# Optimization experiments

Measured on AMD Instinct MI355X. Metric: run time of the kernel, lower is better.

## Reference

```python
import jax, jax.numpy as jnp
import numpy as np

EPS = 1e-5
NUM_HEADS = 16


def layernorm(x, g, b):
    m = jnp.mean(x, axis=-1, keepdims=True)
    v = jnp.mean(jnp.square(x - m), axis=-1, keepdims=True)
    return (x - m) * jax.lax.rsqrt(v + EPS) * g + b


def setup_inputs() -> dict:
    key = jax.random.key(0)
    ks = jax.random.split(key, 8)
    B, S, E, F = 16, 512, 1024, 4096
    s_e = 1.0 / np.sqrt(E)
    s_f = 1.0 / np.sqrt(F)
    return {
        "input": jax.random.normal(ks[0], (B, S, E), jnp.float32),
        "ln1_g": jnp.ones((E,), jnp.float32),
        "ln1_b": jnp.zeros((E,), jnp.float32),
        "wq": jax.random.normal(ks[1], (E, E), jnp.float32) * s_e,
        "bq": jnp.zeros((E,), jnp.float32),
        "wk": jax.random.normal(ks[2], (E, E), jnp.float32) * s_e,
        "bk": jnp.zeros((E,), jnp.float32),
        "wv": jax.random.normal(ks[3], (E, E), jnp.float32) * s_e,
        "bv": jnp.zeros((E,), jnp.float32),
        "wo": jax.random.normal(ks[4], (E, E), jnp.float32) * s_e,
        "bo": jnp.zeros((E,), jnp.float32),
        "ln2_g": jnp.ones((E,), jnp.float32),
        "ln2_b": jnp.zeros((E,), jnp.float32),
        "w1": jax.random.normal(ks[5], (E, F), jnp.float32) * s_e,
        "b1": jnp.zeros((F,), jnp.float32),
        "w2": jax.random.normal(ks[6], (F, E), jnp.float32) * s_f,
        "b2": jnp.zeros((E,), jnp.float32),
    }


def attention(x, wq, bq, wk, bk, wv, bv, wo, bo):
    B, S, E = x.shape
    H = NUM_HEADS
    D = E // H
    q = (x @ wq + bq).reshape(B, S, H, D)
    k = (x @ wk + bk).reshape(B, S, H, D)
    v = (x @ wv + bv).reshape(B, S, H, D)
    scores = jnp.einsum("bqhd,bkhd->bhqk", q, k) * (1.0 / np.sqrt(D))
    attn = jax.nn.softmax(scores, axis=-1)
    out = jnp.einsum("bhqk,bkhd->bqhd", attn, v).reshape(B, S, E)
    return out @ wo + bo


def reference(input, ln1_g, ln1_b, wq, bq, wk, bk, wv, bv, wo, bo,
              ln2_g, ln2_b, w1, b1, w2, b2):
    # pre-LN attention + residual
    x = layernorm(input, ln1_g, ln1_b)
    x = attention(x, wq, bq, wk, bk, wv, bv, wo, bo)
    x = x + input
    # pre-LN MLP (GELU exact, matching nn.GELU default) + residual
    y = layernorm(x, ln2_g, ln2_b)
    y = jax.nn.gelu(y @ w1 + b1, approximate=False)
    y = y @ w2 + b2
    return x + y
```

## Files before the change

kernel.cpp:

```cpp
#include <hip/hip_runtime.h>
#include <hip/hip_bf16.h>


typedef __bf16 bf16x8 __attribute__((ext_vector_type(8)));
typedef __bf16 bf16x4 __attribute__((ext_vector_type(4)));
typedef float  f32x4  __attribute__((ext_vector_type(4)));

#define EPI_QKV  0
#define EPI_RES  1
#define EPI_GELU 2

__device__ __forceinline__ void async_copy16(const void* g, void* l) {
  __builtin_amdgcn_global_load_lds((const __attribute__((address_space(1))) void*)g,
                                   (__attribute__((address_space(3))) void*)l, 16, 0, 0);
}

__global__ __launch_bounds__(256) void prep_weights(
    const float* __restrict__ wq, const float* __restrict__ wk,
    const float* __restrict__ wv, const float* __restrict__ wo,
    const float* __restrict__ w1, const float* __restrict__ w2,
    const float* __restrict__ bq, const float* __restrict__ bk,
    const float* __restrict__ bv,
    __bf16* __restrict__ wqkvT, __bf16* __restrict__ woT,
    __bf16* __restrict__ w1T, __bf16* __restrict__ w2T, float* __restrict__ bqkv) {
  const int bid = blockIdx.x;
  if (bid >= 12288) {
    const int i = (bid - 12288) * 256 + threadIdx.x;
    bqkv[i] = (i < 1024) ? bq[i] : ((i < 2048) ? bk[i - 1024] : bv[i - 2048]);
    return;
  }
  const float* in;
  __bf16* out;
  int K, N, tile;
  if (bid < 4096) {
    const int w = bid >> 10;
    tile = bid & 1023;
    in = (w == 0) ? wq : (w == 1) ? wk : (w == 2) ? wv : wo;
    out = (w == 3) ? woT : (wqkvT + (size_t)w * 1024 * 1024);
    K = 1024; N = 1024;
  } else if (bid < 8192) { tile = bid - 4096; in = w1; out = w1T; K = 1024; N = 4096; }
  else                   { tile = bid - 8192; in = w2; out = w2T; K = 4096; N = 1024; }
  const int ntx = N >> 5;
  const int bx = tile % ntx, by = tile / ntx;
  const int n0 = bx * 32, k0 = by * 32;

  __shared__ float tilebuf[32][33];
  const int tx = threadIdx.x & 31, ty = threadIdx.x >> 5;
#pragma unroll
  for (int i = 0; i < 4; i++)
    tilebuf[ty + i * 8][tx] = in[(size_t)(k0 + ty + i * 8) * N + n0 + tx];
  __syncthreads();
#pragma unroll
  for (int i = 0; i < 4; i++)
    out[(size_t)(n0 + ty + i * 8) * K + k0 + tx] = (__bf16)tilebuf[tx][ty + i * 8];
}

__device__ __forceinline__ float block_sum(float v, float* red) {
#pragma unroll
  for (int off = 32; off; off >>= 1) v += __shfl_down(v, off);
  const int w = threadIdx.x >> 6;
  __syncthreads();
  if ((threadIdx.x & 63) == 0) red[w] = v;
  __syncthreads();
  return red[0] + red[1] + red[2] + red[3];
}

__global__ __launch_bounds__(256) void ln_kernel(const float* __restrict__ x,
                                                 const float* __restrict__ g,
                                                 const float* __restrict__ bta,
                                                 __bf16* __restrict__ out) {
  __shared__ float red[8];
  const int row = blockIdx.x, t = threadIdx.x;
  const float4 v = ((const float4*)(x + (size_t)row * 1024))[t];
  float s = v.x + v.y + v.z + v.w;
  s = block_sum(s, red);
  const float mean = s * (1.0f / 1024.0f);
  const float d0 = v.x - mean, d1 = v.y - mean, d2 = v.z - mean, d3 = v.w - mean;
  float vs = d0 * d0 + d1 * d1 + d2 * d2 + d3 * d3;
  vs = block_sum(vs, red);
  const float rstd = rsqrtf(vs * (1.0f / 1024.0f) + 1e-5f);
  const float4 gg = ((const float4*)g)[t];
  const float4 bb = ((const float4*)bta)[t];
  bf16x4 o;
  o[0] = (__bf16)(d0 * rstd * gg.x + bb.x);
  o[1] = (__bf16)(d1 * rstd * gg.y + bb.y);
  o[2] = (__bf16)(d2 * rstd * gg.z + bb.z);
  o[3] = (__bf16)(d3 * rstd * gg.w + bb.w);
  ((bf16x4*)out)[(size_t)row * 256 + t] = o;
}

template <int EPI>
__global__ __launch_bounds__(256, 2) void gemm_bt(const __bf16* __restrict__ A,
                                                  const __bf16* __restrict__ Bt,
                                                  const float* __restrict__ bias,
                                                  const float* __restrict__ res,
                                                  void* __restrict__ out,
                                                  void* __restrict__ out2,
                                                  int N, int K) {
  __shared__ __bf16 lA[128 * 64];
  __shared__ __bf16 lB[128 * 64];
  const int t = threadIdx.x;
  const int wave = t >> 6, lane = t & 63;
  const int lm = lane & 15, lq = lane >> 4;

  const int Ntiles = gridDim.x;
  const int flat = blockIdx.y * Ntiles + blockIdx.x;
  const int xcd = flat & 7;
  const int local = flat >> 3;
  const int tn = local % Ntiles;
  const int tm = (local / Ntiles) * 8 + xcd;
  const int m0 = tm * 128, n0 = tn * 128;
  const int wm = (wave & 1) * 64, wn = (wave >> 1) * 64;

  f32x4 acc[4][4] = {};

  const int srow = t >> 3, sslot = t & 7;
  const int schunk = sslot ^ (srow & 7);
  const __bf16* aSrc = A + (size_t)(m0 + srow) * K + schunk * 8;
  const __bf16* bSrc = Bt + (size_t)(n0 + srow) * K + schunk * 8;

  for (int k0 = 0; k0 < K; k0 += 64) {
#pragma unroll
    for (int i = 0; i < 4; i++) {
      async_copy16(aSrc + (size_t)(i * 32) * K, lA + i * 2048 + t * 8);
      async_copy16(bSrc + (size_t)(i * 32) * K, lB + i * 2048 + t * 8);
    }
    aSrc += 64; bSrc += 64;
    __syncthreads();
#pragma unroll
    for (int kk = 0; kk < 2; kk++) {
      bf16x8 af[4], bf[4];
      const int slot = (kk * 4 + lq) ^ (lm & 7);
#pragma unroll
      for (int i = 0; i < 4; i++) {
        af[i] = *(const bf16x8*)&lA[(wm + i * 16 + lm) * 64 + slot * 8];
        bf[i] = *(const bf16x8*)&lB[(wn + i * 16 + lm) * 64 + slot * 8];
      }
#pragma unroll
      for (int mi = 0; mi < 4; mi++)
#pragma unroll
        for (int ni = 0; ni < 4; ni++)
          acc[mi][ni] = __builtin_amdgcn_mfma_f32_16x16x32_bf16(af[mi], bf[ni], acc[mi][ni], 0, 0, 0);
    }
    __syncthreads();
  }

#pragma unroll
  for (int mi = 0; mi < 4; mi++) {
    const int gr = m0 + wm + mi * 16 + lq * 4;
#pragma unroll
    for (int ni = 0; ni < 4; ni++) {
      const int gc = n0 + wn + ni * 16 + lm;
      const float bv = bias[gc];
#pragma unroll
      for (int r = 0; r < 4; r++) {
        float v = acc[mi][ni][r] + bv;
        const int row = gr + r;
        if (EPI == EPI_GELU) {
          v = 0.5f * v * (1.0f + erff(v * 0.70710678118654752f));
          ((__bf16*)out)[(size_t)row * N + gc] = (__bf16)v;
        } else if (EPI == EPI_RES) {
          ((float*)out)[(size_t)row * N + gc] = v + res[(size_t)row * N + gc];
        } else {
          if (gc < 2048) {
            ((__bf16*)out)[(size_t)row * 2048 + gc] = (__bf16)v;
          } else {
            const int d = gc & 63, hh = (gc - 2048) >> 6;
            const int bb = row >> 9, ss = row & 511;
            ((__bf16*)out2)[(((size_t)bb * 16 + hh) * 64 + d) * 512 + ss] = (__bf16)v;
          }
        }
      }
    }
  }
}

#define MFMA_QUAD(MI0)                                                         \
  do {                                                                         \
    _Pragma("unroll") for (int kk = 0; kk < 2; ++kk) {                         \
      _Pragma("unroll") for (int ni = 0; ni < 4; ++ni) {                       \
        acc[MI0][ni] = __builtin_amdgcn_mfma_f32_16x16x32_bf16(                \
            af[MI0][kk], bf[ni][kk], acc[MI0][ni], 0, 0, 0);                   \
        acc[(MI0) + 1][ni] = __builtin_amdgcn_mfma_f32_16x16x32_bf16(          \
            af[(MI0) + 1][kk], bf[ni][kk], acc[(MI0) + 1][ni], 0, 0, 0);       \
      }                                                                        \
    }                                                                          \
  } while (0)

#define READ_A(MI)                                                             \
  _Pragma("unroll") for (int kk = 0; kk < 2; ++kk)                             \
      af[MI][kk] = *(const bf16x8*)&bufA[(wm * 128 + (MI)*16 + lm) * 64 +      \
                                         (((kk * 4 + lq) ^ sw) * 8)];

template <int EPI>
__global__ __launch_bounds__(512, 2) void gemm8_bt(const __bf16* __restrict__ A,
                                                   const __bf16* __restrict__ Bt,
                                                   const float* __restrict__ bias,
                                                   void* __restrict__ out,
                                                   void* __restrict__ out2,
                                                   int N, int K) {
  __shared__ __bf16 lA[2 * 256 * 64];
  __shared__ __bf16 lB[2 * 256 * 64];
  const int t = threadIdx.x;
  const int wave = t >> 6, lane = t & 63;
  const int lm = lane & 15, lq = lane >> 4, sw = lm & 7;
  const int wm = wave >> 2, wn = wave & 3;

  const int Ntiles = gridDim.x;
  const int flat = blockIdx.y * Ntiles + blockIdx.x;
  const int xcd = flat & 7;
  const int local = flat >> 3;
  const int tn = local % Ntiles;
  const int tm = (local / Ntiles) * 8 + xcd;
  const int m0 = tm * 256, n0 = tn * 256;

  const int NT = K >> 6;

  const int srow = t >> 3;
  const int schunk = (t & 7) ^ (srow & 7);
  const __bf16* aBase = A + (size_t)(m0 + srow) * K + schunk * 8;
  const __bf16* bBase = Bt + (size_t)(n0 + srow) * K + schunk * 8;
  __bf16* ldA = lA + t * 8;
  __bf16* ldB = lB + t * 8;

  auto stage = [&](int h) {
    if (h >= 4 * NT) return;
    const int tau = h >> 2, type = h & 3, hf = type & 1;
    const size_t roff = (size_t)(hf * 128) * K + (size_t)tau * 64;
    const int loff = (tau & 1) * 16384 + hf * 8192;
    if (type < 2) {
      async_copy16(aBase + roff, ldA + loff);
      async_copy16(aBase + roff + (size_t)64 * K, ldA + loff + 4096);
    } else {
      async_copy16(bBase + roff, ldB + loff);
      async_copy16(bBase + roff + (size_t)64 * K, ldB + loff + 4096);
    }
  };

  f32x4 acc[8][4] = {};

  for (int h = 0; h < 6; ++h) stage(h);
  asm volatile("s_waitcnt vmcnt(4)" ::: "memory");
  __builtin_amdgcn_s_barrier();

  for (int tt = 0; tt < NT; ++tt) {
    const __bf16* bufA = lA + (tt & 1) * 16384;
    const __bf16* bufB = lB + (tt & 1) * 16384;
    bf16x8 af[8][2], bf[4][2];

#pragma unroll
    for (int ni = 0; ni < 4; ++ni)
#pragma unroll
      for (int kk = 0; kk < 2; ++kk)
        bf[ni][kk] = *(const bf16x8*)&bufB[(wn * 64 + ni * 16 + lm) * 64 +
                                           (((kk * 4 + lq) ^ sw) * 8)];
    READ_A(0)
    READ_A(1)
    stage(4 * tt + 6);
    __builtin_amdgcn_s_barrier();
    asm volatile("s_waitcnt lgkmcnt(0)" ::: "memory");
    __builtin_amdgcn_sched_barrier(0);
    __builtin_amdgcn_s_setprio(1);
    MFMA_QUAD(0);
    __builtin_amdgcn_s_setprio(0);
    __builtin_amdgcn_s_barrier();

    READ_A(2)
    READ_A(3)
    READ_A(4)
    READ_A(5)
    READ_A(6)
    READ_A(7)
    stage(4 * tt + 7);
    __builtin_amdgcn_s_barrier();
    asm volatile("s_waitcnt lgkmcnt(0)" ::: "memory");
    __builtin_amdgcn_sched_barrier(0);
    __builtin_amdgcn_s_setprio(1);
    MFMA_QUAD(2);
    __builtin_amdgcn_s_setprio(0);
    __builtin_amdgcn_s_barrier();

    stage(4 * tt + 8);
    __builtin_amdgcn_s_barrier();
    __builtin_amdgcn_s_setprio(1);
    MFMA_QUAD(4);
    __builtin_amdgcn_s_setprio(0);
    __builtin_amdgcn_s_barrier();

    stage(4 * tt + 9);
    __builtin_amdgcn_s_barrier();
    __builtin_amdgcn_s_setprio(1);
    MFMA_QUAD(6);
    __builtin_amdgcn_s_setprio(0);

    if (tt < NT - 1) {
      if (tt == NT - 2) asm volatile("s_waitcnt vmcnt(0)" ::: "memory");
      else              asm volatile("s_waitcnt vmcnt(4)" ::: "memory");
      __builtin_amdgcn_s_barrier();
    }
  }

#pragma unroll
  for (int mi = 0; mi < 8; ++mi) {
    const int gr = m0 + wm * 128 + mi * 16 + lq * 4;
#pragma unroll
    for (int ni = 0; ni < 4; ++ni) {
      const int gc = n0 + wn * 64 + ni * 16 + lm;
      const float bv = bias[gc];
#pragma unroll
      for (int r = 0; r < 4; ++r) {
        float v = acc[mi][ni][r] + bv;
        const int row = gr + r;
        if (EPI == EPI_GELU) {
          v = 0.5f * v * (1.0f + erff(v * 0.70710678118654752f));
          ((__bf16*)out)[(size_t)row * N + gc] = (__bf16)v;
        } else {
          if (gc < 2048) {
            ((__bf16*)out)[(size_t)row * 2048 + gc] = (__bf16)v;
          } else {
            const int d = gc & 63, hh = (gc - 2048) >> 6;
            const int bb = row >> 9, ss = row & 511;
            ((__bf16*)out2)[(((size_t)bb * 16 + hh) * 64 + d) * 512 + ss] = (__bf16)v;
          }
        }
      }
    }
  }
}

__global__ __launch_bounds__(256) void attn_kernel(const __bf16* __restrict__ qk,
                                                   const __bf16* __restrict__ Vt,
                                                   __bf16* __restrict__ outA) {
  __shared__ __bf16 lK[128 * 64];
  __shared__ __bf16 lV[64 * 128];
  __shared__ __bf16 lP[4][16 * 128];
  const int t = threadIdx.x, wave = t >> 6, lane = t & 63;
  const int lm = lane & 15, lq = lane >> 4;
  const int sw = lm & 7;
  const int flat = blockIdx.x;
  const int xcd = flat & 7, local = flat >> 3;
  const int qt = local & 7;
  const int bh = (local >> 3) * 8 + xcd;
  const int h = bh & 15, b = bh >> 4;
  const int q0 = qt * 64 + wave * 16;

  const size_t qrow = (size_t)(b * 512 + q0 + lm) * 2048 + h * 64;
  bf16x8 aq0 = *(const bf16x8*)&qk[qrow + lq * 8];
  bf16x8 aq1 = *(const bf16x8*)&qk[qrow + 32 + lq * 8];

  float mrow[4] = {-3e38f, -3e38f, -3e38f, -3e38f};
  float lrow[4] = {0.f, 0.f, 0.f, 0.f};
  f32x4 o[4] = {};

  const int krow = t >> 3;
  const int kchunk = (t & 7) ^ (krow & 7);
  const __bf16* kSrc = qk + (size_t)(b * 512 + krow) * 2048 + 1024 + h * 64 + kchunk * 8;
  const int vrow = t >> 4;
  const int vchunk = (t & 15) ^ (vrow & 7);
  const __bf16* vSrc = Vt + ((size_t)bh * 64 + vrow) * 512 + vchunk * 8;

  for (int kt = 0; kt < 4; kt++) {
#pragma unroll
    for (int i = 0; i < 4; i++) {
      async_copy16(kSrc + (size_t)(kt * 128 + i * 32) * 2048, lK + i * 2048 + t * 8);
      async_copy16(vSrc + kt * 128 + (size_t)(i * 16) * 512, lV + i * 2048 + t * 8);
    }
    __syncthreads();

    f32x4 s[8];
#pragma unroll
    for (int ni = 0; ni < 8; ni++) {
      bf16x8 bk0 = *(const bf16x8*)&lK[(ni * 16 + lm) * 64 + ((lq ^ sw) * 8)];
      bf16x8 bk1 = *(const bf16x8*)&lK[(ni * 16 + lm) * 64 + (((4 + lq) ^ sw) * 8)];
      f32x4 z = {};
      z = __builtin_amdgcn_mfma_f32_16x16x32_bf16(aq0, bk0, z, 0, 0, 0);
      z = __builtin_amdgcn_mfma_f32_16x16x32_bf16(aq1, bk1, z, 0, 0, 0);
      s[ni] = z;
    }
#pragma unroll
    for (int ni = 0; ni < 8; ni++)
#pragma unroll
      for (int r = 0; r < 4; r++) s[ni][r] *= 0.125f;

    float mnew[4], alpha[4];
#pragma unroll
    for (int r = 0; r < 4; r++) {
      float mx = s[0][r];
#pragma unroll
      for (int ni = 1; ni < 8; ni++) mx = fmaxf(mx, s[ni][r]);
#pragma unroll
      for (int off = 1; off < 16; off <<= 1) mx = fmaxf(mx, __shfl_xor(mx, off));
      mnew[r] = fmaxf(mrow[r], mx);
      alpha[r] = __expf(mrow[r] - mnew[r]);
      mrow[r] = mnew[r];
    }
    float rs[4] = {0.f, 0.f, 0.f, 0.f};
#pragma unroll
    for (int ni = 0; ni < 8; ni++)
#pragma unroll
      for (int r = 0; r < 4; r++) {
        const float p = __expf(s[ni][r] - mnew[r]);
        s[ni][r] = p;
        rs[r] += p;
      }
#pragma unroll
    for (int r = 0; r < 4; r++) {
#pragma unroll
      for (int off = 1; off < 16; off <<= 1) rs[r] += __shfl_xor(rs[r], off);
      lrow[r] = lrow[r] * alpha[r] + rs[r];
    }

#pragma unroll
    for (int ni = 0; ni < 8; ni++) {
      const int chunk = ni * 2 + (lm >> 3);
#pragma unroll
      for (int r = 0; r < 4; r++) {
        const int q = lq * 4 + r;
        lP[wave][q * 128 + ((chunk ^ (q & 7)) * 8) + (lm & 7)] = (__bf16)s[ni][r];
      }
    }
    asm volatile("s_waitcnt lgkmcnt(0)" ::: "memory");
    bf16x8 ap[4];
#pragma unroll
    for (int kc = 0; kc < 4; kc++)
      ap[kc] = *(const bf16x8*)&lP[wave][lm * 128 + (((kc * 4 + lq) ^ sw) * 8)];

#pragma unroll
    for (int di = 0; di < 4; di++)
#pragma unroll
      for (int r = 0; r < 4; r++) o[di][r] *= alpha[r];

#pragma unroll
    for (int di = 0; di < 4; di++) {
#pragma unroll
      for (int kc = 0; kc < 4; kc++) {
        bf16x8 bv = *(const bf16x8*)&lV[(di * 16 + lm) * 128 + (((kc * 4 + lq) ^ sw) * 8)];
        o[di] = __builtin_amdgcn_mfma_f32_16x16x32_bf16(ap[kc], bv, o[di], 0, 0, 0);
      }
    }
    __syncthreads();
  }

#pragma unroll
  for (int di = 0; di < 4; di++)
#pragma unroll
    for (int r = 0; r < 4; r++) {
      const float v = o[di][r] / lrow[r];
      outA[(size_t)(b * 512 + q0 + lq * 4 + r) * 1024 + h * 64 + di * 16 + lm] = (__bf16)v;
    }
}

extern "C" void kernel_launch(void* const* d_in, const int* in_sizes, int n_in,
                              void* d_out, int out_size, void* d_ws, size_t ws_size,
                              hipStream_t stream) {
  const float* input = (const float*)d_in[0];
  const float* ln1_g = (const float*)d_in[1];
  const float* ln1_b = (const float*)d_in[2];
  const float* wq = (const float*)d_in[3];
  const float* bq = (const float*)d_in[4];
  const float* wk = (const float*)d_in[5];
  const float* bk = (const float*)d_in[6];
  const float* wv = (const float*)d_in[7];
  const float* bv = (const float*)d_in[8];
  const float* wo = (const float*)d_in[9];
  const float* bo = (const float*)d_in[10];
  const float* ln2_g = (const float*)d_in[11];
  const float* ln2_b = (const float*)d_in[12];
  const float* w1 = (const float*)d_in[13];
  const float* b1 = (const float*)d_in[14];
  const float* w2 = (const float*)d_in[15];
  const float* b2 = (const float*)d_in[16];

  char* ws = (char*)d_ws;
  __bf16* wqkvT = (__bf16*)(ws + 0);
  __bf16* woT   = (__bf16*)(ws + ((size_t)6 << 20));
  __bf16* w1T   = (__bf16*)(ws + ((size_t)8 << 20));
  __bf16* w2T   = (__bf16*)(ws + ((size_t)16 << 20));
  __bf16* qkbuf = (__bf16*)(ws + ((size_t)24 << 20));
  __bf16* vtbuf = (__bf16*)(ws + ((size_t)56 << 20));
  __bf16* abuf  = (__bf16*)(ws + ((size_t)72 << 20));
  float*  xbuf  = (float*) (ws + ((size_t)24 << 20));
  __bf16* ylnbuf= (__bf16*)(ws + ((size_t)56 << 20));
  __bf16* hbuf  = (__bf16*)(ws + ((size_t)72 << 20));
  float*  bqkv  = (float*) (ws + ((size_t)136 << 20));

  const dim3 blk(256);
  const dim3 blk8(512);
  prep_weights<<<12300, blk, 0, stream>>>(wq, wk, wv, wo, w1, w2, bq, bk, bv,
                                          wqkvT, woT, w1T, w2T, bqkv);

  ln_kernel<<<8192, blk, 0, stream>>>(input, ln1_g, ln1_b, abuf);
  gemm8_bt<EPI_QKV><<<dim3(12, 32), blk8, 0, stream>>>(abuf, wqkvT, bqkv,
                                                       qkbuf, vtbuf, 3072, 1024);
  attn_kernel<<<2048, blk, 0, stream>>>(qkbuf, vtbuf, abuf);
  gemm_bt<EPI_RES><<<dim3(8, 64), blk, 0, stream>>>(abuf, woT, bo, input,
                                                    xbuf, nullptr, 1024, 1024);
  ln_kernel<<<8192, blk, 0, stream>>>(xbuf, ln2_g, ln2_b, ylnbuf);
  gemm8_bt<EPI_GELU><<<dim3(16, 32), blk8, 0, stream>>>(ylnbuf, w1T, b1,
                                                        hbuf, nullptr, 4096, 1024);
  gemm_bt<EPI_RES><<<dim3(8, 64), blk, 0, stream>>>(hbuf, w2T, b2, xbuf,
                                                    d_out, nullptr, 1024, 4096);
}
```

Baseline: 512.9 us.

## Replace simple GEMM with pipelined 256x128 gemm4 kernel and rebalance gemm8 staging

Adds a new 512-thread gemm4_bt kernel with 256x128 tiles, double-buffered async global-to-LDS loads and phased barriers. It replaces the single-buffered 128x128 gemm_bt for the two residual GEMMs and the gemm8 kernel for the QKV projection. The gemm8 pipeline is also restaged: A tiles now load as a whole two tiles ahead, B halves load interleaved with the compute phases, and A fragment reads are spread evenly across the four phases. The aim is to hide global-load latency and balance LDS reads against MFMA work, at the cost of more LDS per block and fewer blocks in the grid for the N=1024 GEMMs.

```diff
diff --git a/kernel.cpp b/kernel.cpp
--- a/kernel.cpp
+++ b/kernel.cpp
@@ -89,92 +89,6 @@
   ((bf16x4*)out)[(size_t)row * 256 + t] = o;
 }
 
-template <int EPI>
-__global__ __launch_bounds__(256, 2) void gemm_bt(const __bf16* __restrict__ A,
-                                                  const __bf16* __restrict__ Bt,
-                                                  const float* __restrict__ bias,
-                                                  const float* __restrict__ res,
-                                                  void* __restrict__ out,
-                                                  void* __restrict__ out2,
-                                                  int N, int K) {
-  __shared__ __bf16 lA[128 * 64];
-  __shared__ __bf16 lB[128 * 64];
-  const int t = threadIdx.x;
-  const int wave = t >> 6, lane = t & 63;
-  const int lm = lane & 15, lq = lane >> 4;
-
-  const int Ntiles = gridDim.x;
-  const int flat = blockIdx.y * Ntiles + blockIdx.x;
-  const int xcd = flat & 7;
-  const int local = flat >> 3;
-  const int tn = local % Ntiles;
-  const int tm = (local / Ntiles) * 8 + xcd;
-  const int m0 = tm * 128, n0 = tn * 128;
-  const int wm = (wave & 1) * 64, wn = (wave >> 1) * 64;
-
-  f32x4 acc[4][4] = {};
-
-  const int srow = t >> 3, sslot = t & 7;
-  const int schunk = sslot ^ (srow & 7);
-  const __bf16* aSrc = A + (size_t)(m0 + srow) * K + schunk * 8;
-  const __bf16* bSrc = Bt + (size_t)(n0 + srow) * K + schunk * 8;
-
-  for (int k0 = 0; k0 < K; k0 += 64) {
-#pragma unroll
-    for (int i = 0; i < 4; i++) {
-      async_copy16(aSrc + (size_t)(i * 32) * K, lA + i * 2048 + t * 8);
-      async_copy16(bSrc + (size_t)(i * 32) * K, lB + i * 2048 + t * 8);
-    }
-    aSrc += 64; bSrc += 64;
-    __syncthreads();
-#pragma unroll
-    for (int kk = 0; kk < 2; kk++) {
-      bf16x8 af[4], bf[4];
-      const int slot = (kk * 4 + lq) ^ (lm & 7);
-#pragma unroll
-      for (int i = 0; i < 4; i++) {
-        af[i] = *(const bf16x8*)&lA[(wm + i * 16 + lm) * 64 + slot * 8];
-        bf[i] = *(const bf16x8*)&lB[(wn + i * 16 + lm) * 64 + slot * 8];
-      }
-#pragma unroll
-      for (int mi = 0; mi < 4; mi++)
-#pragma unroll
-        for (int ni = 0; ni < 4; ni++)
-          acc[mi][ni] = __builtin_amdgcn_mfma_f32_16x16x32_bf16(af[mi], bf[ni], acc[mi][ni], 0, 0, 0);
-    }
-    __syncthreads();
-  }
-
-#pragma unroll
-  for (int mi = 0; mi < 4; mi++) {
-    const int gr = m0 + wm + mi * 16 + lq * 4;
-#pragma unroll
-    for (int ni = 0; ni < 4; ni++) {
-      const int gc = n0 + wn + ni * 16 + lm;
-      const float bv = bias[gc];
-#pragma unroll
-      for (int r = 0; r < 4; r++) {
-        float v = acc[mi][ni][r] + bv;
-        const int row = gr + r;
-        if (EPI == EPI_GELU) {
-          v = 0.5f * v * (1.0f + erff(v * 0.70710678118654752f));
-          ((__bf16*)out)[(size_t)row * N + gc] = (__bf16)v;
-        } else if (EPI == EPI_RES) {
-          ((float*)out)[(size_t)row * N + gc] = v + res[(size_t)row * N + gc];
-        } else {
-          if (gc < 2048) {
-            ((__bf16*)out)[(size_t)row * 2048 + gc] = (__bf16)v;
-          } else {
-            const int d = gc & 63, hh = (gc - 2048) >> 6;
-            const int bb = row >> 9, ss = row & 511;
-            ((__bf16*)out2)[(((size_t)bb * 16 + hh) * 64 + d) * 512 + ss] = (__bf16)v;
-          }
-        }
-      }
-    }
-  }
-}
-
 #define MFMA_QUAD(MI0)                                                         \
   do {                                                                         \
     _Pragma("unroll") for (int kk = 0; kk < 2; ++kk) {                         \
@@ -187,7 +101,12 @@
     }                                                                          \
   } while (0)
 
-#define READ_A(MI)                                                             \
+#define PHASE_SYNC()                                                           \
+  __builtin_amdgcn_s_barrier();                                                \
+  asm volatile("s_waitcnt lgkmcnt(0)" ::: "memory");                           \
+  __builtin_amdgcn_sched_barrier(0)
+
+#define READ_A8(MI)                                                            \
   _Pragma("unroll") for (int kk = 0; kk < 2; ++kk)                             \
       af[MI][kk] = *(const bf16x8*)&bufA[(wm * 128 + (MI)*16 + lm) * 64 +      \
                                          (((kk * 4 + lq) ^ sw) * 8)];
@@ -220,26 +139,26 @@
   const int schunk = (t & 7) ^ (srow & 7);
   const __bf16* aBase = A + (size_t)(m0 + srow) * K + schunk * 8;
   const __bf16* bBase = Bt + (size_t)(n0 + srow) * K + schunk * 8;
-  __bf16* ldA = lA + t * 8;
-  __bf16* ldB = lB + t * 8;
-
-  auto stage = [&](int h) {
-    if (h >= 4 * NT) return;
-    const int tau = h >> 2, type = h & 3, hf = type & 1;
-    const size_t roff = (size_t)(hf * 128) * K + (size_t)tau * 64;
-    const int loff = (tau & 1) * 16384 + hf * 8192;
-    if (type < 2) {
-      async_copy16(aBase + roff, ldA + loff);
-      async_copy16(aBase + roff + (size_t)64 * K, ldA + loff + 4096);
-    } else {
-      async_copy16(bBase + roff, ldB + loff);
-      async_copy16(bBase + roff + (size_t)64 * K, ldB + loff + 4096);
-    }
+
+  auto stageA = [&](int tau) {
+    if (tau >= NT) return;
+    const __bf16* src = aBase + (size_t)tau * 64;
+    __bf16* dst = lA + (tau & 1) * 16384 + t * 8;
+#pragma unroll
+    for (int i = 0; i < 4; ++i)
+      async_copy16(src + (size_t)(i * 64) * K, dst + i * 4096);
   };
+  auto stageB = [&](int tau, int half) {
+    if (tau >= NT) return;
+    const __bf16* src = bBase + (size_t)tau * 64 + (size_t)(half * 128) * K;
+    __bf16* dst = lB + (tau & 1) * 16384 + half * 8192 + t * 8;
+    async_copy16(src, dst);
+    async_copy16(src + (size_t)64 * K, dst + 4096);
+  };
 
   f32x4 acc[8][4] = {};
 
-  for (int h = 0; h < 6; ++h) stage(h);
+  stageA(0); stageB(0, 0); stageB(0, 1); stageA(1);
   asm volatile("s_waitcnt vmcnt(4)" ::: "memory");
   __builtin_amdgcn_s_barrier();
 
@@ -254,46 +173,42 @@
       for (int kk = 0; kk < 2; ++kk)
         bf[ni][kk] = *(const bf16x8*)&bufB[(wn * 64 + ni * 16 + lm) * 64 +
                                            (((kk * 4 + lq) ^ sw) * 8)];
-    READ_A(0)
-    READ_A(1)
-    stage(4 * tt + 6);
-    __builtin_amdgcn_s_barrier();
-    asm volatile("s_waitcnt lgkmcnt(0)" ::: "memory");
-    __builtin_amdgcn_sched_barrier(0);
+    READ_A8(0)
+    READ_A8(1)
+    stageB(tt + 1, 0);
+    PHASE_SYNC();
     __builtin_amdgcn_s_setprio(1);
     MFMA_QUAD(0);
     __builtin_amdgcn_s_setprio(0);
     __builtin_amdgcn_s_barrier();
 
-    READ_A(2)
-    READ_A(3)
-    READ_A(4)
-    READ_A(5)
-    READ_A(6)
-    READ_A(7)
-    stage(4 * tt + 7);
-    __builtin_amdgcn_s_barrier();
-    asm volatile("s_waitcnt lgkmcnt(0)" ::: "memory");
-    __builtin_amdgcn_sched_barrier(0);
+    READ_A8(2)
+    READ_A8(3)
+    stageB(tt + 1, 1);
+    PHASE_SYNC();
     __builtin_amdgcn_s_setprio(1);
     MFMA_QUAD(2);
     __builtin_amdgcn_s_setprio(0);
     __builtin_amdgcn_s_barrier();
 
-    stage(4 * tt + 8);
-    __builtin_amdgcn_s_barrier();
+    READ_A8(4)
+    READ_A8(5)
+    PHASE_SYNC();
     __builtin_amdgcn_s_setprio(1);
     MFMA_QUAD(4);
     __builtin_amdgcn_s_setprio(0);
     __builtin_amdgcn_s_barrier();
 
-    stage(4 * tt + 9);
-    __builtin_amdgcn_s_barrier();
+    READ_A8(6)
+    READ_A8(7)
+    PHASE_SYNC();
     __builtin_amdgcn_s_setprio(1);
     MFMA_QUAD(6);
     __builtin_amdgcn_s_setprio(0);
+    __builtin_amdgcn_s_barrier();
 
     if (tt < NT - 1) {
+      stageA(tt + 2);
       if (tt == NT - 2) asm volatile("s_waitcnt vmcnt(0)" ::: "memory");
       else              asm volatile("s_waitcnt vmcnt(4)" ::: "memory");
       __builtin_amdgcn_s_barrier();
@@ -314,6 +229,126 @@
         if (EPI == EPI_GELU) {
           v = 0.5f * v * (1.0f + erff(v * 0.70710678118654752f));
           ((__bf16*)out)[(size_t)row * N + gc] = (__bf16)v;
+        } else {
+          if (gc < 2048) {
+            ((__bf16*)out)[(size_t)row * 2048 + gc] = (__bf16)v;
+          } else {
+            const int d = gc & 63, hh = (gc - 2048) >> 6;
+            const int bb = row >> 9, ss = row & 511;
+            ((__bf16*)out2)[(((size_t)bb * 16 + hh) * 64 + d) * 512 + ss] = (__bf16)v;
+          }
+        }
+      }
+    }
+  }
+}
+
+#define READ_A4(MI)                                                            \
+  _Pragma("unroll") for (int kk = 0; kk < 2; ++kk)                             \
+      af[MI][kk] = *(const bf16x8*)&bufA[(wm * 64 + (MI)*16 + lm) * 64 +       \
+                                         (((kk * 4 + lq) ^ sw) * 8)];
+
+template <int EPI>
+__global__ __launch_bounds__(512, 2) void gemm4_bt(const __bf16* __restrict__ A,
+                                                   const __bf16* __restrict__ Bt,
+                                                   const float* __restrict__ bias,
+                                                   const float* __restrict__ res,
+                                                   void* __restrict__ out,
+                                                   void* __restrict__ out2,
+                                                   int N, int K) {
+  __shared__ __bf16 lA[2 * 256 * 64];
+  __shared__ __bf16 lB[2 * 128 * 64];
+  const int t = threadIdx.x;
+  const int wave = t >> 6, lane = t & 63;
+  const int lm = lane & 15, lq = lane >> 4, sw = lm & 7;
+  const int wm = wave >> 1, wn = wave & 1;
+
+  const int Ntiles = gridDim.x;
+  const int flat = blockIdx.y * Ntiles + blockIdx.x;
+  const int xcd = flat & 7;
+  const int local = flat >> 3;
+  const int tn = local % Ntiles;
+  const int tm = (local / Ntiles) * 8 + xcd;
+  const int m0 = tm * 256, n0 = tn * 128;
+
+  const int NT = K >> 6;
+
+  const int srow = t >> 3;
+  const int schunk = (t & 7) ^ (srow & 7);
+  const __bf16* aBase = A + (size_t)(m0 + srow) * K + schunk * 8;
+  const __bf16* bBase = Bt + (size_t)(n0 + srow) * K + schunk * 8;
+
+  auto stageA = [&](int tau) {
+    if (tau >= NT) return;
+    const __bf16* src = aBase + (size_t)tau * 64;
+    __bf16* dst = lA + (tau & 1) * 16384 + t * 8;
+#pragma unroll
+    for (int i = 0; i < 4; ++i)
+      async_copy16(src + (size_t)(i * 64) * K, dst + i * 4096);
+  };
+  auto stageB = [&](int tau) {
+    if (tau >= NT) return;
+    const __bf16* src = bBase + (size_t)tau * 64;
+    __bf16* dst = lB + (tau & 1) * 8192 + t * 8;
+    async_copy16(src, dst);
+    async_copy16(src + (size_t)64 * K, dst + 4096);
+  };
+
+  f32x4 acc[4][4] = {};
+
+  stageA(0); stageB(0); stageA(1);
+  asm volatile("s_waitcnt vmcnt(4)" ::: "memory");
+  __builtin_amdgcn_s_barrier();
+
+  for (int tt = 0; tt < NT; ++tt) {
+    const __bf16* bufA = lA + (tt & 1) * 16384;
+    const __bf16* bufB = lB + (tt & 1) * 8192;
+    bf16x8 af[4][2], bf[4][2];
+
+#pragma unroll
+    for (int ni = 0; ni < 4; ++ni)
+#pragma unroll
+      for (int kk = 0; kk < 2; ++kk)
+        bf[ni][kk] = *(const bf16x8*)&bufB[(wn * 64 + ni * 16 + lm) * 64 +
+                                           (((kk * 4 + lq) ^ sw) * 8)];
+    READ_A4(0)
+    READ_A4(1)
+    stageB(tt + 1);
+    PHASE_SYNC();
+    __builtin_amdgcn_s_setprio(1);
+    MFMA_QUAD(0);
+    __builtin_amdgcn_s_setprio(0);
+    __builtin_amdgcn_s_barrier();
+
+    READ_A4(2)
+    READ_A4(3)
+    PHASE_SYNC();
+    __builtin_amdgcn_s_setprio(1);
+    MFMA_QUAD(2);
+    __builtin_amdgcn_s_setprio(0);
+    __builtin_amdgcn_s_barrier();
+
+    if (tt < NT - 1) {
+      stageA(tt + 2);
+      if (tt == NT - 2) asm volatile("s_waitcnt vmcnt(0)" ::: "memory");
+      else              asm volatile("s_waitcnt vmcnt(4)" ::: "memory");
+      __builtin_amdgcn_s_barrier();
+    }
+  }
+
+#pragma unroll
+  for (int mi = 0; mi < 4; ++mi) {
+    const int gr = m0 + wm * 64 + mi * 16 + lq * 4;
+#pragma unroll
+    for (int ni = 0; ni < 4; ++ni) {
+      const int gc = n0 + wn * 64 + ni * 16 + lm;
+      const float bv = bias[gc];
+#pragma unroll
+      for (int r = 0; r < 4; ++r) {
+        float v = acc[mi][ni][r] + bv;
+        const int row = gr + r;
+        if (EPI == EPI_RES) {
+          ((float*)out)[(size_t)row * N + gc] = v + res[(size_t)row * N + gc];
         } else {
           if (gc < 2048) {
             ((__bf16*)out)[(size_t)row * 2048 + gc] = (__bf16)v;
@@ -490,14 +525,14 @@
                                           wqkvT, woT, w1T, w2T, bqkv);
 
   ln_kernel<<<8192, blk, 0, stream>>>(input, ln1_g, ln1_b, abuf);
-  gemm8_bt<EPI_QKV><<<dim3(12, 32), blk8, 0, stream>>>(abuf, wqkvT, bqkv,
+  gemm4_bt<EPI_QKV><<<dim3(24, 32), blk8, 0, stream>>>(abuf, wqkvT, bqkv, nullptr,
                                                        qkbuf, vtbuf, 3072, 1024);
   attn_kernel<<<2048, blk, 0, stream>>>(qkbuf, vtbuf, abuf);
-  gemm_bt<EPI_RES><<<dim3(8, 64), blk, 0, stream>>>(abuf, woT, bo, input,
-                                                    xbuf, nullptr, 1024, 1024);
+  gemm4_bt<EPI_RES><<<dim3(8, 32), blk8, 0, stream>>>(abuf, woT, bo, input,
+                                                      xbuf, nullptr, 1024, 1024);
   ln_kernel<<<8192, blk, 0, stream>>>(xbuf, ln2_g, ln2_b, ylnbuf);
   gemm8_bt<EPI_GELU><<<dim3(16, 32), blk8, 0, stream>>>(ylnbuf, w1T, b1,
                                                         hbuf, nullptr, 4096, 1024);
-  gemm_bt<EPI_RES><<<dim3(8, 64), blk, 0, stream>>>(hbuf, w2T, b2, xbuf,
-                                                    d_out, nullptr, 1024, 4096);
-}
+  gemm4_bt<EPI_RES><<<dim3(8, 32), blk8, 0, stream>>>(hbuf, w2T, b2, xbuf,
+                                                      d_out, nullptr, 1024, 4096);
+}
```

New measurement: 551.6 us. 1.08x slower.

## Double-buffer LDS in gemm_bt and route QKV projection through it

Applied to the files above, without the earlier changes.

Gives the 128x128 gemm_bt kernel two LDS buffers, so the async global-to-LDS copy of the next K tile is issued before the MFMAs on the current tile, with a waitcnt and barrier per iteration. The QKV projection launch moves from the 256x256 8-wave gemm8_bt to the 128-tile gemm_bt with a larger grid. The goal is to overlap memory loads with compute in the smaller GEMMs. LDS use doubles to 64 KB per block, which can lower occupancy, and the QKV GEMM loses the reuse of the larger tile.

```diff
diff --git a/kernel.cpp b/kernel.cpp
--- a/kernel.cpp
+++ b/kernel.cpp
@@ -97,8 +97,8 @@
                                                   void* __restrict__ out,
                                                   void* __restrict__ out2,
                                                   int N, int K) {
-  __shared__ __bf16 lA[128 * 64];
-  __shared__ __bf16 lB[128 * 64];
+  __shared__ __bf16 lA[2][128 * 64];
+  __shared__ __bf16 lB[2][128 * 64];
   const int t = threadIdx.x;
   const int wave = t >> 6, lane = t & 63;
   const int lm = lane & 15, lq = lane >> 4;
@@ -118,31 +118,46 @@
   const int schunk = sslot ^ (srow & 7);
   const __bf16* aSrc = A + (size_t)(m0 + srow) * K + schunk * 8;
   const __bf16* bSrc = Bt + (size_t)(n0 + srow) * K + schunk * 8;
-
-  for (int k0 = 0; k0 < K; k0 += 64) {
+  const int NT = K >> 6;
+
+  auto stage = [&](int tau) {
+    if (tau >= NT) return;
+    const __bf16* sA = aSrc + (size_t)tau * 64;
+    const __bf16* sB = bSrc + (size_t)tau * 64;
+    __bf16* dA = &lA[tau & 1][t * 8];
+    __bf16* dB = &lB[tau & 1][t * 8];
 #pragma unroll
     for (int i = 0; i < 4; i++) {
-      async_copy16(aSrc + (size_t)(i * 32) * K, lA + i * 2048 + t * 8);
-      async_copy16(bSrc + (size_t)(i * 32) * K, lB + i * 2048 + t * 8);
-    }
-    aSrc += 64; bSrc += 64;
-    __syncthreads();
+      async_copy16(sA + (size_t)(i * 32) * K, dA + i * 2048);
+      async_copy16(sB + (size_t)(i * 32) * K, dB + i * 2048);
+    }
+  };
+
+  stage(0);
+  asm volatile("s_waitcnt vmcnt(0)" ::: "memory");
+  __builtin_amdgcn_s_barrier();
+
+  for (int tt = 0; tt < NT; ++tt) {
+    stage(tt + 1);
+    const __bf16* bufA = lA[tt & 1];
+    const __bf16* bufB = lB[tt & 1];
 #pragma unroll
     for (int kk = 0; kk < 2; kk++) {
-      bf16x8 af[4], bf[4];
+      bf16x8 af[4], bfr[4];
       const int slot = (kk * 4 + lq) ^ (lm & 7);
 #pragma unroll
       for (int i = 0; i < 4; i++) {
-        af[i] = *(const bf16x8*)&lA[(wm + i * 16 + lm) * 64 + slot * 8];
-        bf[i] = *(const bf16x8*)&lB[(wn + i * 16 + lm) * 64 + slot * 8];
+        af[i] = *(const bf16x8*)&bufA[(wm + i * 16 + lm) * 64 + slot * 8];
+        bfr[i] = *(const bf16x8*)&bufB[(wn + i * 16 + lm) * 64 + slot * 8];
       }
 #pragma unroll
       for (int mi = 0; mi < 4; mi++)
 #pragma unroll
         for (int ni = 0; ni < 4; ni++)
-          acc[mi][ni] = __builtin_amdgcn_mfma_f32_16x16x32_bf16(af[mi], bf[ni], acc[mi][ni], 0, 0, 0);
-    }
-    __syncthreads();
+          acc[mi][ni] = __builtin_amdgcn_mfma_f32_16x16x32_bf16(af[mi], bfr[ni], acc[mi][ni], 0, 0, 0);
+    }
+    asm volatile("s_waitcnt vmcnt(0)" ::: "memory");
+    __builtin_amdgcn_s_barrier();
   }
 
 #pragma unroll
@@ -187,7 +202,7 @@
     }                                                                          \
   } while (0)
 
-#define READ_A(MI)                                                             \
+#define READ_A8(MI)                                                            \
   _Pragma("unroll") for (int kk = 0; kk < 2; ++kk)                             \
       af[MI][kk] = *(const bf16x8*)&bufA[(wm * 128 + (MI)*16 + lm) * 64 +      \
                                          (((kk * 4 + lq) ^ sw) * 8)];
@@ -254,8 +269,8 @@
       for (int kk = 0; kk < 2; ++kk)
         bf[ni][kk] = *(const bf16x8*)&bufB[(wn * 64 + ni * 16 + lm) * 64 +
                                            (((kk * 4 + lq) ^ sw) * 8)];
-    READ_A(0)
-    READ_A(1)
+    READ_A8(0)
+    READ_A8(1)
     stage(4 * tt + 6);
     __builtin_amdgcn_s_barrier();
     asm volatile("s_waitcnt lgkmcnt(0)" ::: "memory");
@@ -265,12 +280,12 @@
     __builtin_amdgcn_s_setprio(0);
     __builtin_amdgcn_s_barrier();
 
-    READ_A(2)
-    READ_A(3)
-    READ_A(4)
-    READ_A(5)
-    READ_A(6)
-    READ_A(7)
+    READ_A8(2)
+    READ_A8(3)
+    READ_A8(4)
+    READ_A8(5)
+    READ_A8(6)
+    READ_A8(7)
     stage(4 * tt + 7);
     __builtin_amdgcn_s_barrier();
     asm volatile("s_waitcnt lgkmcnt(0)" ::: "memory");
@@ -490,8 +505,8 @@
                                           wqkvT, woT, w1T, w2T, bqkv);
 
   ln_kernel<<<8192, blk, 0, stream>>>(input, ln1_g, ln1_b, abuf);
-  gemm8_bt<EPI_QKV><<<dim3(12, 32), blk8, 0, stream>>>(abuf, wqkvT, bqkv,
-                                                       qkbuf, vtbuf, 3072, 1024);
+  gemm_bt<EPI_QKV><<<dim3(24, 64), blk, 0, stream>>>(abuf, wqkvT, bqkv, nullptr,
+                                                     qkbuf, vtbuf, 3072, 1024);
   attn_kernel<<<2048, blk, 0, stream>>>(qkbuf, vtbuf, abuf);
   gemm_bt<EPI_RES><<<dim3(8, 64), blk, 0, stream>>>(abuf, woT, bo, input,
                                                     xbuf, nullptr, 1024, 1024);
```

Result: faster. 502.5 us (-2.0%).
